# Kernel tuning notes

Hardware: AMD Instinct MI355X
Metric: run time of the kernel (lower is better)

The kernel has to match this reference:

```python
import jax, jax.numpy as jnp
import numpy as np

B, N, C = 32, 577, 1024
NUM_HEADS = 16
HEAD_DIM = C // NUM_HEADS
SCALE = HEAD_DIM ** -0.5
HW = 24          # sqrt(N-1)
POOL = 8         # AdaptiveAvgPool2d output size
KS = HW // POOL  # exact 3x3 average pooling


def setup_inputs() -> dict:
    key = jax.random.key(0)
    k1, k2, k3 = jax.random.split(key, 3)
    X = jax.random.normal(k1, (B, N, C), dtype=jnp.float32)
    W_qkv = jax.random.normal(k2, (3 * C, C), dtype=jnp.float32) * (C ** -0.5)
    W_proj = jax.random.normal(k3, (C, C), dtype=jnp.float32) * (C ** -0.5)
    b_proj = jnp.zeros((C,), dtype=jnp.float32)
    return {"X": X, "W_qkv": W_qkv, "W_proj": W_proj, "b_proj": b_proj, "layer_idx": 1}


def reference(X, W_qkv, W_proj, b_proj, layer_idx):
    # layer_idx <= 100 branch: two-stage pooled-query attention
    qkv = X @ W_qkv.T                              # [B, N, 3C]
    Xq, Xk, Xv = jnp.split(qkv, 3, axis=-1)        # each [B, N, C]

    # Adaptive avg-pool the non-cls query tokens to an 8x8 grid (exact 3x3 mean)
    Qp = Xq[:, :-1, :].reshape(B, POOL, KS, POOL, KS, C).mean(axis=(2, 4))  # [B,8,8,C]
    Qp = Qp.reshape(B, POOL * POOL, C)             # [B, 64, C]

    def to_heads(t, L):
        return t.reshape(B, L, NUM_HEADS, HEAD_DIM).transpose(0, 2, 1, 3)

    Qh = to_heads(Xq, N)       # [B, H, N, d]
    Kh = to_heads(Xk, N)
    Vh = to_heads(Xv, N)
    Q = to_heads(Qp, POOL * POOL)  # [B, H, 64, d]

    # Stage 1: pooled queries cross-attend to full K/V
    s1 = jnp.einsum('bhqd,bhkd->bhqk', Q * SCALE, Kh)   # [B,H,64,N]
    A1 = jax.nn.softmax(s1, axis=-1)
    Q_delta = jnp.einsum('bhqk,bhkd->bhqd', A1, Vh)     # [B,H,64,d]

    # Stage 2: original queries attend to pooled queries, read Q_delta
    s2 = jnp.einsum('bhnd,bhqd->bhnq', Qh * SCALE, Q)   # [B,H,N,64]
    A2 = jax.nn.softmax(s2, axis=-1)
    out = jnp.einsum('bhnq,bhqd->bhnd', A2, Q_delta)    # [B,H,N,d]

    out = out.transpose(0, 2, 1, 3).reshape(B, N, C)
    return out @ W_proj.T + b_proj
```

## Files before the change

### kernel.cpp

```cpp
#include <hip/hip_runtime.h>

typedef unsigned short u16;
typedef u16 u16x8 __attribute__((ext_vector_type(8)));
typedef u16 u16x4 __attribute__((ext_vector_type(4)));
typedef __bf16 bf16x8 __attribute__((ext_vector_type(8)));
typedef float f32x4 __attribute__((ext_vector_type(4)));

#define DEVI static __device__ __forceinline__

#define BB 32
#define NN 577
#define CC 1024
#define HH 16
#define DD 64
#define MM (BB * NN)
#define SCALE_ 0.125f

DEVI u16 f2bf(float f) {
  union { float f; unsigned u; } v; v.f = f;
  unsigned r = v.u + 0x7FFFu + ((v.u >> 16) & 1u);
  return (u16)(r >> 16);
}
DEVI float bf2f(u16 b) {
  union { unsigned u; float f; } v; v.u = ((unsigned)b) << 16; return v.f;
}
DEVI f32x4 mfma16(u16x8 a, u16x8 b, f32x4 c) {
  return __builtin_amdgcn_mfma_f32_16x16x32_bf16(
      __builtin_bit_cast(bf16x8, a), __builtin_bit_cast(bf16x8, b), c, 0, 0, 0);
}
DEVI void gload_lds16(const u16* g, u16* l) {
  __builtin_amdgcn_global_load_lds(
      (const __attribute__((address_space(1))) void*)g,
      (__attribute__((address_space(3))) void*)l, 16, 0, 0);
}

__global__ void cvt_kernel(const float* __restrict__ in, u16* __restrict__ out, int n4) {
  int i = blockIdx.x * blockDim.x + threadIdx.x;
  int stride = gridDim.x * blockDim.x;
  for (; i < n4; i += stride) {
    float4 v = ((const float4*)in)[i];
    u16x4 o = { f2bf(v.x), f2bf(v.y), f2bf(v.z), f2bf(v.w) };
    ((u16x4*)out)[i] = o;
  }
}

__global__ __launch_bounds__(256) void gemm_bt2(
    const u16* __restrict__ A, const u16* __restrict__ Bw,
    u16* __restrict__ Cb, float* __restrict__ Cf, const float* __restrict__ bias,
    int M, int N, int K, int MT, int NT)
{
  __shared__ u16 Als[128 * 64];
  __shared__ u16 Bls[128 * 64];

  int nwg = MT * NT;
  int orig = blockIdx.x;
  int q = nwg >> 3, r = nwg & 7;
  int xcd = orig & 7, idx = orig >> 3;
  int wg = (xcd < r ? xcd * (q + 1) : r * (q + 1) + (xcd - r) * q) + idx;
  int mt = wg / NT, nt = wg % NT;

  const int t = threadIdx.x, lane = t & 63, w = t >> 6;
  const int wr = (w >> 1) * 64, wc = (w & 1) * 64;
  const int fr = lane & 15, fg = lane >> 4;
  const int m0 = mt * 128, n0 = nt * 128;
  f32x4 acc[4][4] = {};

  const int swcol = ((lane & 7) ^ ((lane >> 3) & 7)) * 8;
  const u16* pA[4];
  const u16* pB[4];
#pragma unroll
  for (int i = 0; i < 4; ++i) {
    int row = w * 32 + i * 8 + (lane >> 3);
    int ga = m0 + row; if (ga > M - 1) ga = M - 1;
    pA[i] = A + (size_t)ga * K + swcol;
    pB[i] = Bw + (size_t)(n0 + row) * K + swcol;
  }

  for (int kt = 0; kt < K; kt += 64) {
#pragma unroll
    for (int i = 0; i < 4; ++i) {
      int c = w * 4 + i;
      gload_lds16(pA[i] + kt, &Als[c * 512]);
      gload_lds16(pB[i] + kt, &Bls[c * 512]);
    }
    __syncthreads();
#pragma unroll
    for (int kk = 0; kk < 2; ++kk) {
      u16x8 af[4], bfr[4];
#pragma unroll
      for (int m = 0; m < 4; ++m) {
        int row = wr + m * 16 + fr;
        int ch = (kk * 4 + fg) ^ (fr & 7);
        af[m] = *(const u16x8*)&Als[row * 64 + ch * 8];
      }
#pragma unroll
      for (int n = 0; n < 4; ++n) {
        int row = wc + n * 16 + fr;
        int ch = (kk * 4 + fg) ^ (fr & 7);
        bfr[n] = *(const u16x8*)&Bls[row * 64 + ch * 8];
      }
#pragma unroll
      for (int m = 0; m < 4; ++m)
#pragma unroll
        for (int n = 0; n < 4; ++n)
          acc[m][n] = mfma16(af[m], bfr[n], acc[m][n]);
    }
    __syncthreads();
  }

#pragma unroll
  for (int m = 0; m < 4; ++m) {
#pragma unroll
    for (int j = 0; j < 4; ++j) {
      int row = m0 + wr + m * 16 + fg * 4 + j;
      if (row >= M) continue;
#pragma unroll
      for (int n = 0; n < 4; ++n) {
        int col = n0 + wc + n * 16 + fr;
        float v = acc[m][n][j];
        if (Cf) Cf[(size_t)row * N + col] = v + bias[col];
        else    Cb[(size_t)row * N + col] = f2bf(v);
      }
    }
  }
}

__global__ __launch_bounds__(256) void pool_kernel(const u16* __restrict__ qkv, u16* __restrict__ Qp) {
  int b = blockIdx.x >> 6, pq = blockIdx.x & 63;
  int py = pq >> 3, px = pq & 7;
  int c0 = threadIdx.x * 4;
  float s0 = 0.f, s1 = 0.f, s2 = 0.f, s3 = 0.f;
#pragma unroll
  for (int dy = 0; dy < 3; ++dy)
#pragma unroll
    for (int dx = 0; dx < 3; ++dx) {
      int n = (py * 3 + dy) * 24 + px * 3 + dx;
      u16x4 v = *(const u16x4*)(qkv + (size_t)(b * NN + n) * 3072 + c0);
      s0 += bf2f(v[0]); s1 += bf2f(v[1]); s2 += bf2f(v[2]); s3 += bf2f(v[3]);
    }
  const float r = 1.f / 9.f;
  u16x4 o = { f2bf(s0 * r), f2bf(s1 * r), f2bf(s2 * r), f2bf(s3 * r) };
  *(u16x4*)(Qp + (size_t)(b * 64 + pq) * CC + c0) = o;
}

__global__ __launch_bounds__(256) void stage1_kernel(
    const u16* __restrict__ qkv, const u16* __restrict__ Qp, u16* __restrict__ QdT)
{
  __shared__ u16 Kls[64][72];
  __shared__ u16 Vt[64][72];
  __shared__ u16 Pls[4][16][72];
  int bh = blockIdx.x, b = bh >> 4, h = bh & 15;
  int t = threadIdx.x, lane = t & 63, w = t >> 6;
  int fr = lane & 15, fg = lane >> 4;

  const u16* Qb = Qp + (size_t)(b * 64 + w * 16 + fr) * CC + h * DD;
  u16x8 qf0 = *(const u16x8*)(Qb + fg * 8);
  u16x8 qf1 = *(const u16x8*)(Qb + 32 + fg * 8);

  f32x4 o[4] = {};
  float rowm[4] = {-1e30f, -1e30f, -1e30f, -1e30f};
  float rowl[4] = {};

  for (int kt = 0; kt < 10; ++kt) {
#pragma unroll
    for (int i = 0; i < 2; ++i) {
      int g = t + i * 256;
      int key = g >> 3, cc = (g & 7) * 8;
      int n = kt * 64 + key;
      u16x8 kv = {}, vv = {};
      if (n < NN) {
        const u16* p = qkv + (size_t)(b * NN + n) * 3072 + h * DD + cc;
        kv = *(const u16x8*)(p + CC);
        vv = *(const u16x8*)(p + 2 * CC);
      }
      *(u16x8*)&Kls[key][cc] = kv;
#pragma unroll
      for (int j = 0; j < 8; ++j) Vt[cc + j][key] = vv[j];
    }
    __syncthreads();

    f32x4 s[4] = {};
#pragma unroll
    for (int kk = 0; kk < 2; ++kk) {
      u16x8 qf = kk ? qf1 : qf0;
#pragma unroll
      for (int n = 0; n < 4; ++n) {
        u16x8 kf = *(const u16x8*)&Kls[n * 16 + fr][kk * 32 + fg * 8];
        s[n] = mfma16(qf, kf, s[n]);
      }
    }
    float mx[4] = {-1e30f, -1e30f, -1e30f, -1e30f};
#pragma unroll
    for (int n = 0; n < 4; ++n) {
      int key = kt * 64 + n * 16 + fr;
#pragma unroll
      for (int j = 0; j < 4; ++j) {
        float v = s[n][j] * SCALE_;
        if (key >= NN) v = -1e30f;
        s[n][j] = v;
        mx[j] = fmaxf(mx[j], v);
      }
    }
    for (int d = 1; d < 16; d <<= 1) {
#pragma unroll
      for (int j = 0; j < 4; ++j) mx[j] = fmaxf(mx[j], __shfl_xor(mx[j], d));
    }
    float corr[4];
#pragma unroll
    for (int j = 0; j < 4; ++j) {
      float mn = fmaxf(rowm[j], mx[j]);
      corr[j] = __expf(rowm[j] - mn);
      rowm[j] = mn;
    }
    float rs[4] = {};
#pragma unroll
    for (int n = 0; n < 4; ++n)
#pragma unroll
      for (int j = 0; j < 4; ++j) {
        float p = __expf(s[n][j] - rowm[j]);
        s[n][j] = p;
        rs[j] += p;
      }
    for (int d = 1; d < 16; d <<= 1) {
#pragma unroll
      for (int j = 0; j < 4; ++j) rs[j] += __shfl_xor(rs[j], d);
    }
#pragma unroll
    for (int j = 0; j < 4; ++j) rowl[j] = rowl[j] * corr[j] + rs[j];
#pragma unroll
    for (int n = 0; n < 4; ++n)
#pragma unroll
      for (int j = 0; j < 4; ++j) o[n][j] *= corr[j];

#pragma unroll
    for (int n = 0; n < 4; ++n)
#pragma unroll
      for (int j = 0; j < 4; ++j)
        Pls[w][fg * 4 + j][n * 16 + fr] = f2bf(s[n][j]);
    __syncthreads();

#pragma unroll
    for (int kk = 0; kk < 2; ++kk) {
      u16x8 pf = *(const u16x8*)&Pls[w][fr][kk * 32 + fg * 8];
#pragma unroll
      for (int n = 0; n < 4; ++n) {
        u16x8 vf = *(const u16x8*)&Vt[n * 16 + fr][kk * 32 + fg * 8];
        o[n] = mfma16(pf, vf, o[n]);
      }
    }
    __syncthreads();
  }

#pragma unroll
  for (int n = 0; n < 4; ++n)
#pragma unroll
    for (int j = 0; j < 4; ++j) {
      int dv = n * 16 + fr, q2 = w * 16 + fg * 4 + j;
      QdT[((size_t)bh * 64 + dv) * 64 + q2] = f2bf(o[n][j] / rowl[j]);
    }
}

__global__ __launch_bounds__(256) void stage2_kernel(
    const u16* __restrict__ qkv, const u16* __restrict__ Qp,
    const u16* __restrict__ QdT, u16* __restrict__ AO)
{
  __shared__ u16 Qpl[64][72];
  __shared__ u16 Qdl[64][72];
  __shared__ u16 Pls[4][16][72];
  int id = blockIdx.x;
  int ntile = id % 10;
  int bh = id / 10, b = bh >> 4, h = bh & 15;
  int t = threadIdx.x, lane = t & 63, w = t >> 6;
  int fr = lane & 15, fg = lane >> 4;

#pragma unroll
  for (int i = 0; i < 2; ++i) {
    int g = t + i * 256;
    int row = g >> 3, cc = (g & 7) * 8;
    *(u16x8*)&Qpl[row][cc] = *(const u16x8*)(Qp + (size_t)(b * 64 + row) * CC + h * DD + cc);
    *(u16x8*)&Qdl[row][cc] = *(const u16x8*)(QdT + ((size_t)bh * 64 + row) * 64 + cc);
  }
  __syncthreads();

  int n0 = ntile * 64;
  int qrow = n0 + w * 16 + fr;
  int qc = qrow < NN ? qrow : NN - 1;
  const u16* Qb = qkv + (size_t)(b * NN + qc) * 3072 + h * DD;
  u16x8 qf0 = *(const u16x8*)(Qb + fg * 8);
  u16x8 qf1 = *(const u16x8*)(Qb + 32 + fg * 8);

  f32x4 s[4] = {};
#pragma unroll
  for (int kk = 0; kk < 2; ++kk) {
    u16x8 qf = kk ? qf1 : qf0;
#pragma unroll
    for (int n = 0; n < 4; ++n) {
      u16x8 bfrag = *(const u16x8*)&Qpl[n * 16 + fr][kk * 32 + fg * 8];
      s[n] = mfma16(qf, bfrag, s[n]);
    }
  }
  float mx[4] = {-1e30f, -1e30f, -1e30f, -1e30f};
#pragma unroll
  for (int n = 0; n < 4; ++n)
#pragma unroll
    for (int j = 0; j < 4; ++j) {
      float v = s[n][j] * SCALE_;
      s[n][j] = v;
      mx[j] = fmaxf(mx[j], v);
    }
  for (int d = 1; d < 16; d <<= 1) {
#pragma unroll
    for (int j = 0; j < 4; ++j) mx[j] = fmaxf(mx[j], __shfl_xor(mx[j], d));
  }
  float rs[4] = {};
#pragma unroll
  for (int n = 0; n < 4; ++n)
#pragma unroll
    for (int j = 0; j < 4; ++j) {
      float p = __expf(s[n][j] - mx[j]);
      s[n][j] = p;
      rs[j] += p;
    }
  for (int d = 1; d < 16; d <<= 1) {
#pragma unroll
    for (int j = 0; j < 4; ++j) rs[j] += __shfl_xor(rs[j], d);
  }

#pragma unroll
  for (int n = 0; n < 4; ++n)
#pragma unroll
    for (int j = 0; j < 4; ++j)
      Pls[w][fg * 4 + j][n * 16 + fr] = f2bf(s[n][j]);
  __syncthreads();

  f32x4 of[4] = {};
#pragma unroll
  for (int kk = 0; kk < 2; ++kk) {
    u16x8 pf = *(const u16x8*)&Pls[w][fr][kk * 32 + fg * 8];
#pragma unroll
    for (int n = 0; n < 4; ++n) {
      u16x8 qd = *(const u16x8*)&Qdl[n * 16 + fr][kk * 32 + fg * 8];
      of[n] = mfma16(pf, qd, of[n]);
    }
  }

#pragma unroll
  for (int n = 0; n < 4; ++n)
#pragma unroll
    for (int j = 0; j < 4; ++j) {
      int orow = n0 + w * 16 + fg * 4 + j;
      if (orow < NN)
        AO[(size_t)(b * NN + orow) * CC + h * DD + n * 16 + fr] = f2bf(of[n][j] / rs[j]);
    }
}

extern "C" void kernel_launch(void* const* d_in, const int* in_sizes, int n_in,
                              void* d_out, int out_size, void* d_ws, size_t ws_size,
                              hipStream_t stream) {
  const float* X     = (const float*)d_in[0];
  const float* Wqkv  = (const float*)d_in[1];
  const float* Wproj = (const float*)d_in[2];
  const float* bproj = (const float*)d_in[3];

  char* ws = (char*)d_ws;
  u16* Xb  = (u16*)(ws + 0);
  u16* Wqb = (u16*)(ws + 37814272);
  u16* Wpb = (u16*)(ws + 44105728);
  u16* qkv = (u16*)(ws + 46202880);
  u16* Qpb = (u16*)(ws + 159645696);
  u16* QdT = (u16*)(ws + 163840000);
  u16* AO  = (u16*)(ws + 168034304);

  cvt_kernel<<<2048, 256, 0, stream>>>(X, Xb, (BB * NN * CC) / 4);
  cvt_kernel<<<1024, 256, 0, stream>>>(Wqkv, Wqb, (3 * CC * CC) / 4);
  cvt_kernel<<<512, 256, 0, stream>>>(Wproj, Wpb, (CC * CC) / 4);

  gemm_bt2<<<145 * 24, 256, 0, stream>>>(Xb, Wqb, qkv, nullptr, nullptr,
                                         MM, 3 * CC, CC, 145, 24);

  pool_kernel<<<BB * 64, 256, 0, stream>>>(qkv, Qpb);
  stage1_kernel<<<BB * HH, 256, 0, stream>>>(qkv, Qpb, QdT);
  stage2_kernel<<<BB * HH * 10, 256, 0, stream>>>(qkv, Qpb, QdT, AO);

  gemm_bt2<<<145 * 8, 256, 0, stream>>>(AO, Wpb, nullptr, (float*)d_out, bproj,
                                        MM, CC, CC, 145, 8);
}
```

Before: 302.2 us.

## Double-buffer GEMM with 256x128 tiles, 512 threads, and interleaved prefetch

Replaces the 128x128 single-buffered GEMM with a 256x128 tile computed by 8 waves. LDS is double-buffered, and the global-to-LDS loads for the next k-tile are issued between MFMA groups, with s_setprio raising priority around the MFMA bursts. Each k-step now needs one barrier instead of two, and the larger tile should improve reuse of B and overlap memory with compute. The trade-offs are more LDS use (96KB), fewer workgroups, and tile padding at the M edge (73*256 versus 18464 rows).

After: 383.8 us. +27.0%, slower.

```diff
diff --git a/kernel.cpp b/kernel.cpp
--- a/kernel.cpp
+++ b/kernel.cpp
@@ -44,13 +44,13 @@
   }
 }
 
-__global__ __launch_bounds__(256) void gemm_bt2(
+__global__ __launch_bounds__(512) void gemm_p2(
     const u16* __restrict__ A, const u16* __restrict__ Bw,
     u16* __restrict__ Cb, float* __restrict__ Cf, const float* __restrict__ bias,
     int M, int N, int K, int MT, int NT)
 {
-  __shared__ u16 Als[128 * 64];
-  __shared__ u16 Bls[128 * 64];
+  __shared__ u16 Als[2][256 * 64];
+  __shared__ u16 Bls[2][128 * 64];
 
   int nwg = MT * NT;
   int orig = blockIdx.x;
@@ -60,63 +60,107 @@
   int mt = wg / NT, nt = wg % NT;
 
   const int t = threadIdx.x, lane = t & 63, w = t >> 6;
-  const int wr = (w >> 1) * 64, wc = (w & 1) * 64;
+  const int wr2 = w >> 2, wc2 = w & 3;
   const int fr = lane & 15, fg = lane >> 4;
-  const int m0 = mt * 128, n0 = nt * 128;
-  f32x4 acc[4][4] = {};
+  const int m0 = mt * 256, n0 = nt * 128;
+
+  f32x4 acc[8][2] = {};
 
   const int swcol = ((lane & 7) ^ ((lane >> 3) & 7)) * 8;
   const u16* pA[4];
-  const u16* pB[4];
+  const u16* pB[2];
 #pragma unroll
   for (int i = 0; i < 4; ++i) {
-    int row = w * 32 + i * 8 + (lane >> 3);
+    int row = i * 64 + w * 8 + (lane >> 3);
     int ga = m0 + row; if (ga > M - 1) ga = M - 1;
     pA[i] = A + (size_t)ga * K + swcol;
+  }
+#pragma unroll
+  for (int i = 0; i < 2; ++i) {
+    int row = i * 64 + w * 8 + (lane >> 3);
     pB[i] = Bw + (size_t)(n0 + row) * K + swcol;
   }
 
-  for (int kt = 0; kt < K; kt += 64) {
-#pragma unroll
-    for (int i = 0; i < 4; ++i) {
-      int c = w * 4 + i;
-      gload_lds16(pA[i] + kt, &Als[c * 512]);
-      gload_lds16(pB[i] + kt, &Bls[c * 512]);
+#pragma unroll
+  for (int i = 0; i < 4; ++i) gload_lds16(pA[i], &Als[0][i * 4096 + w * 512]);
+#pragma unroll
+  for (int i = 0; i < 2; ++i) gload_lds16(pB[i], &Bls[0][i * 4096 + w * 512]);
+  __syncthreads();
+
+  const int c0 = (fg ^ (fr & 7)) * 8;
+  const int c1 = ((4 + fg) ^ (fr & 7)) * 8;
+  const int nkt = K >> 6;
+
+  for (int tk = 0; tk < nkt; ++tk) {
+    const int cur = tk & 1, nxt = cur ^ 1;
+    const u16* Ac = &Als[cur][0];
+    const u16* Bc = &Bls[cur][0];
+    const int ktn = (tk + 1) << 6;
+    const bool more = (tk + 1 < nkt);
+
+    if (more) {
+      gload_lds16(pA[0] + ktn, &Als[nxt][0 * 4096 + w * 512]);
+      gload_lds16(pA[1] + ktn, &Als[nxt][1 * 4096 + w * 512]);
+      gload_lds16(pA[2] + ktn, &Als[nxt][2 * 4096 + w * 512]);
+    }
+    u16x8 b00 = *(const u16x8*)&Bc[(wc2 * 32 +  0 + fr) * 64 + c0];
+    u16x8 b01 = *(const u16x8*)&Bc[(wc2 * 32 + 16 + fr) * 64 + c0];
+    u16x8 b10 = *(const u16x8*)&Bc[(wc2 * 32 +  0 + fr) * 64 + c1];
+    u16x8 b11 = *(const u16x8*)&Bc[(wc2 * 32 + 16 + fr) * 64 + c1];
+    {
+      u16x8 a0[4], a1[4];
+#pragma unroll
+      for (int m = 0; m < 4; ++m) {
+        int row = wr2 * 128 + m * 16 + fr;
+        a0[m] = *(const u16x8*)&Ac[row * 64 + c0];
+        a1[m] = *(const u16x8*)&Ac[row * 64 + c1];
+      }
+      __builtin_amdgcn_s_setprio(1);
+#pragma unroll
+      for (int m = 0; m < 4; ++m) {
+        acc[m][0] = mfma16(a0[m], b00, acc[m][0]);
+        acc[m][1] = mfma16(a0[m], b01, acc[m][1]);
+        acc[m][0] = mfma16(a1[m], b10, acc[m][0]);
+        acc[m][1] = mfma16(a1[m], b11, acc[m][1]);
+      }
+      __builtin_amdgcn_s_setprio(0);
+    }
+
+    if (more) {
+      gload_lds16(pA[3] + ktn, &Als[nxt][3 * 4096 + w * 512]);
+      gload_lds16(pB[0] + ktn, &Bls[nxt][0 * 4096 + w * 512]);
+      gload_lds16(pB[1] + ktn, &Bls[nxt][1 * 4096 + w * 512]);
+    }
+    {
+      u16x8 a0[4], a1[4];
+#pragma unroll
+      for (int m = 0; m < 4; ++m) {
+        int row = wr2 * 128 + (m + 4) * 16 + fr;
+        a0[m] = *(const u16x8*)&Ac[row * 64 + c0];
+        a1[m] = *(const u16x8*)&Ac[row * 64 + c1];
+      }
+      __builtin_amdgcn_s_setprio(1);
+#pragma unroll
+      for (int m = 0; m < 4; ++m) {
+        acc[m + 4][0] = mfma16(a0[m], b00, acc[m + 4][0]);
+        acc[m + 4][1] = mfma16(a0[m], b01, acc[m + 4][1]);
+        acc[m + 4][0] = mfma16(a1[m], b10, acc[m + 4][0]);
+        acc[m + 4][1] = mfma16(a1[m], b11, acc[m + 4][1]);
+      }
+      __builtin_amdgcn_s_setprio(0);
     }
     __syncthreads();
-#pragma unroll
-    for (int kk = 0; kk < 2; ++kk) {
-      u16x8 af[4], bfr[4];
-#pragma unroll
-      for (int m = 0; m < 4; ++m) {
-        int row = wr + m * 16 + fr;
-        int ch = (kk * 4 + fg) ^ (fr & 7);
-        af[m] = *(const u16x8*)&Als[row * 64 + ch * 8];
-      }
-#pragma unroll
-      for (int n = 0; n < 4; ++n) {
-        int row = wc + n * 16 + fr;
-        int ch = (kk * 4 + fg) ^ (fr & 7);
-        bfr[n] = *(const u16x8*)&Bls[row * 64 + ch * 8];
-      }
-#pragma unroll
-      for (int m = 0; m < 4; ++m)
-#pragma unroll
-        for (int n = 0; n < 4; ++n)
-          acc[m][n] = mfma16(af[m], bfr[n], acc[m][n]);
-    }
-    __syncthreads();
-  }
-
-#pragma unroll
-  for (int m = 0; m < 4; ++m) {
-#pragma unroll
-    for (int j = 0; j < 4; ++j) {
-      int row = m0 + wr + m * 16 + fg * 4 + j;
+  }
+
+#pragma unroll
+  for (int m = 0; m < 8; ++m) {
+#pragma unroll
+    for (int j = 0; j < 4; ++j) {
+      int row = m0 + wr2 * 128 + m * 16 + fg * 4 + j;
       if (row >= M) continue;
 #pragma unroll
-      for (int n = 0; n < 4; ++n) {
-        int col = n0 + wc + n * 16 + fr;
+      for (int n = 0; n < 2; ++n) {
+        int col = n0 + wc2 * 32 + n * 16 + fr;
         float v = acc[m][n][j];
         if (Cf) Cf[(size_t)row * N + col] = v + bias[col];
         else    Cb[(size_t)row * N + col] = f2bf(v);
@@ -375,13 +419,13 @@
   cvt_kernel<<<1024, 256, 0, stream>>>(Wqkv, Wqb, (3 * CC * CC) / 4);
   cvt_kernel<<<512, 256, 0, stream>>>(Wproj, Wpb, (CC * CC) / 4);
 
-  gemm_bt2<<<145 * 24, 256, 0, stream>>>(Xb, Wqb, qkv, nullptr, nullptr,
-                                         MM, 3 * CC, CC, 145, 24);
+  gemm_p2<<<73 * 24, 512, 0, stream>>>(Xb, Wqb, qkv, nullptr, nullptr,
+                                       MM, 3 * CC, CC, 73, 24);
 
   pool_kernel<<<BB * 64, 256, 0, stream>>>(qkv, Qpb);
   stage1_kernel<<<BB * HH, 256, 0, stream>>>(qkv, Qpb, QdT);
   stage2_kernel<<<BB * HH * 10, 256, 0, stream>>>(qkv, Qpb, QdT, AO);
 
-  gemm_bt2<<<145 * 8, 256, 0, stream>>>(AO, Wpb, nullptr, (float*)d_out, bproj,
-                                        MM, CC, CC, 145, 8);
-}
+  gemm_p2<<<73 * 8, 512, 0, stream>>>(AO, Wpb, nullptr, (float*)d_out, bproj,
+                                      MM, CC, CC, 73, 8);
+}
```

## Replace QKV GEMM with 256x256-tile, 8-wave, four-slot pipelined kernel

Applied to the files above, without the earlier changes.

Adds a new bf16 GEMM for the QKV projection. It uses 256x256 output tiles with 512 threads and a four-slot LDS ring fed by direct global-to-LDS loads, split into half-K stages. MFMA bursts are interleaved with prefetches under explicit barriers and raised wave priority. The goal is more data reuse per tile and better overlap of loads with compute than the previous 128x128 kernel. The cost is large accumulator register pressure, 64KB of LDS per block and fewer blocks. The last row tile is padded, with out-of-range rows clamped on load and skipped on store.

Result: no change. 300.4 us (-0.6%).

```diff
diff --git a/kernel.cpp b/kernel.cpp
--- a/kernel.cpp
+++ b/kernel.cpp
@@ -33,6 +33,11 @@
       (const __attribute__((address_space(1))) void*)g,
       (__attribute__((address_space(3))) void*)l, 16, 0, 0);
 }
+DEVI void bar() {
+  __builtin_amdgcn_sched_barrier(0);
+  __builtin_amdgcn_s_barrier();
+  __builtin_amdgcn_sched_barrier(0);
+}
 
 __global__ void cvt_kernel(const float* __restrict__ in, u16* __restrict__ out, int n4) {
   int i = blockIdx.x * blockDim.x + threadIdx.x;
@@ -41,6 +46,141 @@
     float4 v = ((const float4*)in)[i];
     u16x4 o = { f2bf(v.x), f2bf(v.y), f2bf(v.z), f2bf(v.w) };
     ((u16x4*)out)[i] = o;
+  }
+}
+
+__global__ __launch_bounds__(512, 2) void gemm_p4(
+    const u16* __restrict__ A, const u16* __restrict__ Bw,
+    u16* __restrict__ Cb, int M, int N, int K, int MT, int NT)
+{
+  __shared__ u16 Als[4][8192];
+  __shared__ u16 Bls[4][8192];
+
+  int nwg = MT * NT;
+  int orig = blockIdx.x;
+  int q = nwg >> 3, r = nwg & 7;
+  int xcd = orig & 7, idx = orig >> 3;
+  int wg = (xcd < r ? xcd * (q + 1) : r * (q + 1) + (xcd - r) * q) + idx;
+  int mt = wg / NT, nt = wg % NT;
+
+  const int t = threadIdx.x, lane = t & 63, w = t >> 6;
+  const int wr2 = w >> 2, wc2 = w & 3;
+  const int fr = lane & 15, fg = lane >> 4;
+  const int m0 = mt * 256, n0 = nt * 256;
+
+  f32x4 acc[8][4] = {};
+
+  const int srccol = ((lane & 3) ^ ((lane >> 3) & 3)) * 8;
+  int rA0 = m0 + w * 16 + (lane >> 2);
+  int rA1 = rA0 + 128;
+  if (rA0 > M - 1) rA0 = M - 1;
+  if (rA1 > M - 1) rA1 = M - 1;
+  const u16* pA0 = A + (size_t)rA0 * K + srccol;
+  const u16* pA1 = A + (size_t)rA1 * K + srccol;
+  const u16* pB0 = Bw + (size_t)(n0 + w * 16 + (lane >> 2)) * K + srccol;
+  const u16* pB1 = pB0 + (size_t)128 * K;
+  const int ldsoff = w * 512;
+
+  auto stageA = [&](int tile, int kh, int slot) {
+    const int col = tile * 64 + kh * 32;
+    gload_lds16(pA0 + col, &Als[slot][ldsoff]);
+    gload_lds16(pA1 + col, &Als[slot][4096 + ldsoff]);
+  };
+  auto stageB = [&](int tile, int kh, int slot) {
+    const int col = tile * 64 + kh * 32;
+    gload_lds16(pB0 + col, &Bls[slot][ldsoff]);
+    gload_lds16(pB1 + col, &Bls[slot][4096 + ldsoff]);
+  };
+
+  const int swch8 = (fg ^ ((fr >> 1) & 3)) * 8;
+  const int aoff = (wr2 * 128 + fr) * 32 + swch8;
+  const int boff = (wc2 * 64 + fr) * 32 + swch8;
+
+  const int nkt = K >> 6;
+
+  stageA(0, 0, 0); stageB(0, 0, 0);
+  stageA(0, 1, 1); stageB(0, 1, 1);
+  stageA(1, 0, 2); stageB(1, 0, 2);
+  asm volatile("s_waitcnt vmcnt(8)" ::: "memory");
+  bar();
+
+  for (int tk = 0; tk < nkt; ++tk) {
+    const int s0 = (2 * tk) & 3, s1 = (2 * tk + 1) & 3, s3 = (2 * tk + 3) & 3;
+    const int t1 = (tk + 1 < nkt) ? tk + 1 : 0;
+    const int t2 = (tk + 2 < nkt) ? tk + 2 : tk + 2 - nkt;
+    u16x8 a[4], b[4];
+
+#pragma unroll
+    for (int m = 0; m < 4; ++m) a[m] = *(const u16x8*)&Als[s0][aoff + m * 512];
+#pragma unroll
+    for (int n = 0; n < 4; ++n) b[n] = *(const u16x8*)&Bls[s0][boff + n * 512];
+    stageA(t1, 1, s3);
+    bar();
+    __builtin_amdgcn_s_setprio(1);
+#pragma unroll
+    for (int m = 0; m < 4; ++m)
+#pragma unroll
+      for (int n = 0; n < 4; ++n)
+        acc[m][n] = mfma16(a[m], b[n], acc[m][n]);
+    __builtin_amdgcn_s_setprio(0);
+    bar();
+
+#pragma unroll
+    for (int m = 0; m < 4; ++m) a[m] = *(const u16x8*)&Als[s0][aoff + (m + 4) * 512];
+    stageB(t1, 1, s3);
+    bar();
+    __builtin_amdgcn_s_setprio(1);
+#pragma unroll
+    for (int m = 0; m < 4; ++m)
+#pragma unroll
+      for (int n = 0; n < 4; ++n)
+        acc[m + 4][n] = mfma16(a[m], b[n], acc[m + 4][n]);
+    __builtin_amdgcn_s_setprio(0);
+    asm volatile("s_waitcnt vmcnt(8)" ::: "memory");
+    bar();
+
+#pragma unroll
+    for (int m = 0; m < 4; ++m) a[m] = *(const u16x8*)&Als[s1][aoff + m * 512];
+#pragma unroll
+    for (int n = 0; n < 4; ++n) b[n] = *(const u16x8*)&Bls[s1][boff + n * 512];
+    stageA(t2, 0, s0);
+    bar();
+    __builtin_amdgcn_s_setprio(1);
+#pragma unroll
+    for (int m = 0; m < 4; ++m)
+#pragma unroll
+      for (int n = 0; n < 4; ++n)
+        acc[m][n] = mfma16(a[m], b[n], acc[m][n]);
+    __builtin_amdgcn_s_setprio(0);
+    bar();
+
+#pragma unroll
+    for (int m = 0; m < 4; ++m) a[m] = *(const u16x8*)&Als[s1][aoff + (m + 4) * 512];
+    stageB(t2, 0, s0);
+    bar();
+    __builtin_amdgcn_s_setprio(1);
+#pragma unroll
+    for (int m = 0; m < 4; ++m)
+#pragma unroll
+      for (int n = 0; n < 4; ++n)
+        acc[m + 4][n] = mfma16(a[m], b[n], acc[m + 4][n]);
+    __builtin_amdgcn_s_setprio(0);
+    asm volatile("s_waitcnt vmcnt(8)" ::: "memory");
+    bar();
+  }
+
+#pragma unroll
+  for (int m = 0; m < 8; ++m) {
+#pragma unroll
+    for (int j = 0; j < 4; ++j) {
+      int row = m0 + wr2 * 128 + m * 16 + fg * 4 + j;
+      if (row >= M) continue;
+#pragma unroll
+      for (int n = 0; n < 4; ++n) {
+        int col = n0 + wc2 * 64 + n * 16 + fr;
+        Cb[(size_t)row * N + col] = f2bf(acc[m][n][j]);
+      }
+    }
   }
 }
 
@@ -375,8 +515,7 @@
   cvt_kernel<<<1024, 256, 0, stream>>>(Wqkv, Wqb, (3 * CC * CC) / 4);
   cvt_kernel<<<512, 256, 0, stream>>>(Wproj, Wpb, (CC * CC) / 4);
 
-  gemm_bt2<<<145 * 24, 256, 0, stream>>>(Xb, Wqb, qkv, nullptr, nullptr,
-                                         MM, 3 * CC, CC, 145, 24);
+  gemm_p4<<<73 * 12, 512, 0, stream>>>(Xb, Wqb, qkv, MM, 3 * CC, CC, 73, 12);
 
   pool_kernel<<<BB * 64, 256, 0, stream>>>(qkv, Qpb);
   stage1_kernel<<<BB * HH, 256, 0, stream>>>(qkv, Qpb, QdT);
```

## Fuse pooling, stage-1 and stage-2 attention into one per-head kernel; merge conversions

Applied to the files above, without the earlier changes.

Pooling, stage-1 cross-attention and stage-2 attention now run in one kernel, one block per (batch, head). Pooled queries and Q_delta stay in shared memory instead of going through global buffers, which removes two launches and the intermediate global traffic. The three fp32-to-bf16 conversion launches are merged into a single grid-stride kernel. In exchange, stage 2 runs serially in 10 tiles inside 512 blocks rather than across 5120 blocks, which lowers parallelism for that phase.

After: 298.3 us. No clear change (-1.3%).

```diff
diff --git a/kernel.cpp b/kernel.cpp
--- a/kernel.cpp
+++ b/kernel.cpp
@@ -34,13 +34,23 @@
       (__attribute__((address_space(3))) void*)l, 16, 0, 0);
 }
 
-__global__ void cvt_kernel(const float* __restrict__ in, u16* __restrict__ out, int n4) {
+__global__ void cvt3_kernel(const float* __restrict__ X, const float* __restrict__ Wq,
+                            const float* __restrict__ Wp, u16* __restrict__ Xb,
+                            u16* __restrict__ Wqb, u16* __restrict__ Wpb) {
+  const int nX = (MM * CC) / 4;
+  const int nQ = (3 * CC * CC) / 4;
+  const int nP = (CC * CC) / 4;
+  const int total = nX + nQ + nP;
   int i = blockIdx.x * blockDim.x + threadIdx.x;
   int stride = gridDim.x * blockDim.x;
-  for (; i < n4; i += stride) {
-    float4 v = ((const float4*)in)[i];
+  for (; i < total; i += stride) {
+    const float* in; u16* out; int k;
+    if (i < nX)            { in = X;  out = Xb;  k = i; }
+    else if (i < nX + nQ)  { in = Wq; out = Wqb; k = i - nX; }
+    else                   { in = Wp; out = Wpb; k = i - nX - nQ; }
+    float4 v = ((const float4*)in)[k];
     u16x4 o = { f2bf(v.x), f2bf(v.y), f2bf(v.z), f2bf(v.w) };
-    ((u16x4*)out)[i] = o;
+    ((u16x4*)out)[k] = o;
   }
 }
 
@@ -125,99 +135,191 @@
   }
 }
 
-__global__ __launch_bounds__(256) void pool_kernel(const u16* __restrict__ qkv, u16* __restrict__ Qp) {
-  int b = blockIdx.x >> 6, pq = blockIdx.x & 63;
-  int py = pq >> 3, px = pq & 7;
-  int c0 = threadIdx.x * 4;
-  float s0 = 0.f, s1 = 0.f, s2 = 0.f, s3 = 0.f;
-#pragma unroll
-  for (int dy = 0; dy < 3; ++dy)
-#pragma unroll
-    for (int dx = 0; dx < 3; ++dx) {
-      int n = (py * 3 + dy) * 24 + px * 3 + dx;
-      u16x4 v = *(const u16x4*)(qkv + (size_t)(b * NN + n) * 3072 + c0);
-      s0 += bf2f(v[0]); s1 += bf2f(v[1]); s2 += bf2f(v[2]); s3 += bf2f(v[3]);
-    }
-  const float r = 1.f / 9.f;
-  u16x4 o = { f2bf(s0 * r), f2bf(s1 * r), f2bf(s2 * r), f2bf(s3 * r) };
-  *(u16x4*)(Qp + (size_t)(b * 64 + pq) * CC + c0) = o;
-}
-
-__global__ __launch_bounds__(256) void stage1_kernel(
-    const u16* __restrict__ qkv, const u16* __restrict__ Qp, u16* __restrict__ QdT)
+__global__ __launch_bounds__(256) void attn_fused(
+    const u16* __restrict__ qkv, u16* __restrict__ AO)
 {
+  __shared__ u16 Qp[64][72];
+  __shared__ u16 Qd[64][72];
   __shared__ u16 Kls[64][72];
   __shared__ u16 Vt[64][72];
   __shared__ u16 Pls[4][16][72];
+
   int bh = blockIdx.x, b = bh >> 4, h = bh & 15;
   int t = threadIdx.x, lane = t & 63, w = t >> 6;
   int fr = lane & 15, fg = lane >> 4;
 
-  const u16* Qb = Qp + (size_t)(b * 64 + w * 16 + fr) * CC + h * DD;
-  u16x8 qf0 = *(const u16x8*)(Qb + fg * 8);
-  u16x8 qf1 = *(const u16x8*)(Qb + 32 + fg * 8);
-
-  f32x4 o[4] = {};
-  float rowm[4] = {-1e30f, -1e30f, -1e30f, -1e30f};
-  float rowl[4] = {};
-
-  for (int kt = 0; kt < 10; ++kt) {
-#pragma unroll
-    for (int i = 0; i < 2; ++i) {
-      int g = t + i * 256;
-      int key = g >> 3, cc = (g & 7) * 8;
-      int n = kt * 64 + key;
-      u16x8 kv = {}, vv = {};
-      if (n < NN) {
-        const u16* p = qkv + (size_t)(b * NN + n) * 3072 + h * DD + cc;
-        kv = *(const u16x8*)(p + CC);
-        vv = *(const u16x8*)(p + 2 * CC);
-      }
-      *(u16x8*)&Kls[key][cc] = kv;
-#pragma unroll
-      for (int j = 0; j < 8; ++j) Vt[cc + j][key] = vv[j];
-    }
-    __syncthreads();
+  {
+    int pq = t >> 2, d0 = (t & 3) * 16;
+    int py = pq >> 3, px = pq & 7;
+    float s[16] = {};
+#pragma unroll
+    for (int dy = 0; dy < 3; ++dy)
+#pragma unroll
+      for (int dx = 0; dx < 3; ++dx) {
+        int n = (py * 3 + dy) * 24 + px * 3 + dx;
+        const u16* p = qkv + (size_t)(b * NN + n) * 3072 + h * DD + d0;
+        u16x8 v0 = *(const u16x8*)p;
+        u16x8 v1 = *(const u16x8*)(p + 8);
+#pragma unroll
+        for (int j = 0; j < 8; ++j) { s[j] += bf2f(v0[j]); s[8 + j] += bf2f(v1[j]); }
+      }
+    const float rinv = 1.f / 9.f;
+    u16x8 o0, o1;
+#pragma unroll
+    for (int j = 0; j < 8; ++j) { o0[j] = f2bf(s[j] * rinv); o1[j] = f2bf(s[8 + j] * rinv); }
+    *(u16x8*)&Qp[pq][d0] = o0;
+    *(u16x8*)&Qp[pq][d0 + 8] = o1;
+  }
+  __syncthreads();
+
+  {
+    u16x8 qf0 = *(const u16x8*)&Qp[w * 16 + fr][fg * 8];
+    u16x8 qf1 = *(const u16x8*)&Qp[w * 16 + fr][32 + fg * 8];
+
+    f32x4 o[4] = {};
+    float rowm[4] = {-1e30f, -1e30f, -1e30f, -1e30f};
+    float rowl[4] = {};
+
+    for (int kt = 0; kt < 10; ++kt) {
+#pragma unroll
+      for (int i = 0; i < 2; ++i) {
+        int g = t + i * 256;
+        int key = g >> 3, cc = (g & 7) * 8;
+        int n = kt * 64 + key;
+        u16x8 kv = {}, vv = {};
+        if (n < NN) {
+          const u16* p = qkv + (size_t)(b * NN + n) * 3072 + h * DD + cc;
+          kv = *(const u16x8*)(p + CC);
+          vv = *(const u16x8*)(p + 2 * CC);
+        }
+        *(u16x8*)&Kls[key][cc] = kv;
+#pragma unroll
+        for (int j = 0; j < 8; ++j) Vt[cc + j][key] = vv[j];
+      }
+      __syncthreads();
+
+      f32x4 s[4] = {};
+#pragma unroll
+      for (int kk = 0; kk < 2; ++kk) {
+        u16x8 qf = kk ? qf1 : qf0;
+#pragma unroll
+        for (int n = 0; n < 4; ++n) {
+          u16x8 kf = *(const u16x8*)&Kls[n * 16 + fr][kk * 32 + fg * 8];
+          s[n] = mfma16(qf, kf, s[n]);
+        }
+      }
+      float mx[4] = {-1e30f, -1e30f, -1e30f, -1e30f};
+#pragma unroll
+      for (int n = 0; n < 4; ++n) {
+        int key = kt * 64 + n * 16 + fr;
+#pragma unroll
+        for (int j = 0; j < 4; ++j) {
+          float v = s[n][j] * SCALE_;
+          if (key >= NN) v = -1e30f;
+          s[n][j] = v;
+          mx[j] = fmaxf(mx[j], v);
+        }
+      }
+      for (int d = 1; d < 16; d <<= 1) {
+#pragma unroll
+        for (int j = 0; j < 4; ++j) mx[j] = fmaxf(mx[j], __shfl_xor(mx[j], d));
+      }
+      float corr[4];
+#pragma unroll
+      for (int j = 0; j < 4; ++j) {
+        float mn = fmaxf(rowm[j], mx[j]);
+        corr[j] = __expf(rowm[j] - mn);
+        rowm[j] = mn;
+      }
+      float rs[4] = {};
+#pragma unroll
+      for (int n = 0; n < 4; ++n)
+#pragma unroll
+        for (int j = 0; j < 4; ++j) {
+          float p = __expf(s[n][j] - rowm[j]);
+          s[n][j] = p;
+          rs[j] += p;
+        }
+      for (int d = 1; d < 16; d <<= 1) {
+#pragma unroll
+        for (int j = 0; j < 4; ++j) rs[j] += __shfl_xor(rs[j], d);
+      }
+#pragma unroll
+      for (int j = 0; j < 4; ++j) rowl[j] = rowl[j] * corr[j] + rs[j];
+#pragma unroll
+      for (int n = 0; n < 4; ++n)
+#pragma unroll
+        for (int j = 0; j < 4; ++j) o[n][j] *= corr[j];
+
+#pragma unroll
+      for (int n = 0; n < 4; ++n)
+#pragma unroll
+        for (int j = 0; j < 4; ++j)
+          Pls[w][fg * 4 + j][n * 16 + fr] = f2bf(s[n][j]);
+      __syncthreads();
+
+#pragma unroll
+      for (int kk = 0; kk < 2; ++kk) {
+        u16x8 pf = *(const u16x8*)&Pls[w][fr][kk * 32 + fg * 8];
+#pragma unroll
+        for (int n = 0; n < 4; ++n) {
+          u16x8 vf = *(const u16x8*)&Vt[n * 16 + fr][kk * 32 + fg * 8];
+          o[n] = mfma16(pf, vf, o[n]);
+        }
+      }
+      __syncthreads();
+    }
+
+#pragma unroll
+    for (int n = 0; n < 4; ++n)
+#pragma unroll
+      for (int j = 0; j < 4; ++j)
+        Qd[n * 16 + fr][w * 16 + fg * 4 + j] = f2bf(o[n][j] / rowl[j]);
+  }
+  __syncthreads();
+
+  u16x8 bq[2][4], dq[2][4];
+#pragma unroll
+  for (int kk = 0; kk < 2; ++kk)
+#pragma unroll
+    for (int n = 0; n < 4; ++n) {
+      bq[kk][n] = *(const u16x8*)&Qp[n * 16 + fr][kk * 32 + fg * 8];
+      dq[kk][n] = *(const u16x8*)&Qd[n * 16 + fr][kk * 32 + fg * 8];
+    }
+
+  for (int nt = 0; nt < 10; ++nt) {
+    int n0 = nt * 64;
+    int qrow = n0 + w * 16 + fr;
+    int qc = qrow < NN ? qrow : NN - 1;
+    const u16* Qb = qkv + (size_t)(b * NN + qc) * 3072 + h * DD;
+    u16x8 a0 = *(const u16x8*)(Qb + fg * 8);
+    u16x8 a1 = *(const u16x8*)(Qb + 32 + fg * 8);
 
     f32x4 s[4] = {};
 #pragma unroll
-    for (int kk = 0; kk < 2; ++kk) {
-      u16x8 qf = kk ? qf1 : qf0;
-#pragma unroll
-      for (int n = 0; n < 4; ++n) {
-        u16x8 kf = *(const u16x8*)&Kls[n * 16 + fr][kk * 32 + fg * 8];
-        s[n] = mfma16(qf, kf, s[n]);
-      }
+    for (int n = 0; n < 4; ++n) {
+      s[n] = mfma16(a0, bq[0][n], s[n]);
+      s[n] = mfma16(a1, bq[1][n], s[n]);
     }
     float mx[4] = {-1e30f, -1e30f, -1e30f, -1e30f};
 #pragma unroll
-    for (int n = 0; n < 4; ++n) {
-      int key = kt * 64 + n * 16 + fr;
+    for (int n = 0; n < 4; ++n)
 #pragma unroll
       for (int j = 0; j < 4; ++j) {
         float v = s[n][j] * SCALE_;
-        if (key >= NN) v = -1e30f;
         s[n][j] = v;
         mx[j] = fmaxf(mx[j], v);
       }
-    }
     for (int d = 1; d < 16; d <<= 1) {
 #pragma unroll
       for (int j = 0; j < 4; ++j) mx[j] = fmaxf(mx[j], __shfl_xor(mx[j], d));
     }
-    float corr[4];
-#pragma unroll
-    for (int j = 0; j < 4; ++j) {
-      float mn = fmaxf(rowm[j], mx[j]);
-      corr[j] = __expf(rowm[j] - mn);
-      rowm[j] = mn;
-    }
     float rs[4] = {};
 #pragma unroll
     for (int n = 0; n < 4; ++n)
 #pragma unroll
       for (int j = 0; j < 4; ++j) {
-        float p = __expf(s[n][j] - rowm[j]);
+        float p = __expf(s[n][j] - mx[j]);
         s[n][j] = p;
         rs[j] += p;
       }
@@ -225,12 +327,6 @@
 #pragma unroll
       for (int j = 0; j < 4; ++j) rs[j] += __shfl_xor(rs[j], d);
     }
-#pragma unroll
-    for (int j = 0; j < 4; ++j) rowl[j] = rowl[j] * corr[j] + rs[j];
-#pragma unroll
-    for (int n = 0; n < 4; ++n)
-#pragma unroll
-      for (int j = 0; j < 4; ++j) o[n][j] *= corr[j];
 
 #pragma unroll
     for (int n = 0; n < 4; ++n)
@@ -239,119 +335,25 @@
         Pls[w][fg * 4 + j][n * 16 + fr] = f2bf(s[n][j]);
     __syncthreads();
 
+    f32x4 of[4] = {};
 #pragma unroll
     for (int kk = 0; kk < 2; ++kk) {
       u16x8 pf = *(const u16x8*)&Pls[w][fr][kk * 32 + fg * 8];
 #pragma unroll
-      for (int n = 0; n < 4; ++n) {
-        u16x8 vf = *(const u16x8*)&Vt[n * 16 + fr][kk * 32 + fg * 8];
-        o[n] = mfma16(pf, vf, o[n]);
-      }
-    }
+      for (int n = 0; n < 4; ++n)
+        of[n] = mfma16(pf, dq[kk][n], of[n]);
+    }
+
+#pragma unroll
+    for (int n = 0; n < 4; ++n)
+#pragma unroll
+      for (int j = 0; j < 4; ++j) {
+        int orow = n0 + w * 16 + fg * 4 + j;
+        if (orow < NN)
+          AO[(size_t)(b * NN + orow) * CC + h * DD + n * 16 + fr] = f2bf(of[n][j] / rs[j]);
+      }
     __syncthreads();
   }
-
-#pragma unroll
-  for (int n = 0; n < 4; ++n)
-#pragma unroll
-    for (int j = 0; j < 4; ++j) {
-      int dv = n * 16 + fr, q2 = w * 16 + fg * 4 + j;
-      QdT[((size_t)bh * 64 + dv) * 64 + q2] = f2bf(o[n][j] / rowl[j]);
-    }
-}
-
-__global__ __launch_bounds__(256) void stage2_kernel(
-    const u16* __restrict__ qkv, const u16* __restrict__ Qp,
-    const u16* __restrict__ QdT, u16* __restrict__ AO)
-{
-  __shared__ u16 Qpl[64][72];
-  __shared__ u16 Qdl[64][72];
-  __shared__ u16 Pls[4][16][72];
-  int id = blockIdx.x;
-  int ntile = id % 10;
-  int bh = id / 10, b = bh >> 4, h = bh & 15;
-  int t = threadIdx.x, lane = t & 63, w = t >> 6;
-  int fr = lane & 15, fg = lane >> 4;
-
-#pragma unroll
-  for (int i = 0; i < 2; ++i) {
-    int g = t + i * 256;
-    int row = g >> 3, cc = (g & 7) * 8;
-    *(u16x8*)&Qpl[row][cc] = *(const u16x8*)(Qp + (size_t)(b * 64 + row) * CC + h * DD + cc);
-    *(u16x8*)&Qdl[row][cc] = *(const u16x8*)(QdT + ((size_t)bh * 64 + row) * 64 + cc);
-  }
-  __syncthreads();
-
-  int n0 = ntile * 64;
-  int qrow = n0 + w * 16 + fr;
-  int qc = qrow < NN ? qrow : NN - 1;
-  const u16* Qb = qkv + (size_t)(b * NN + qc) * 3072 + h * DD;
-  u16x8 qf0 = *(const u16x8*)(Qb + fg * 8);
-  u16x8 qf1 = *(const u16x8*)(Qb + 32 + fg * 8);
-
-  f32x4 s[4] = {};
-#pragma unroll
-  for (int kk = 0; kk < 2; ++kk) {
-    u16x8 qf = kk ? qf1 : qf0;
-#pragma unroll
-    for (int n = 0; n < 4; ++n) {
-      u16x8 bfrag = *(const u16x8*)&Qpl[n * 16 + fr][kk * 32 + fg * 8];
-      s[n] = mfma16(qf, bfrag, s[n]);
-    }
-  }
-  float mx[4] = {-1e30f, -1e30f, -1e30f, -1e30f};
-#pragma unroll
-  for (int n = 0; n < 4; ++n)
-#pragma unroll
-    for (int j = 0; j < 4; ++j) {
-      float v = s[n][j] * SCALE_;
-      s[n][j] = v;
-      mx[j] = fmaxf(mx[j], v);
-    }
-  for (int d = 1; d < 16; d <<= 1) {
-#pragma unroll
-    for (int j = 0; j < 4; ++j) mx[j] = fmaxf(mx[j], __shfl_xor(mx[j], d));
-  }
-  float rs[4] = {};
-#pragma unroll
-  for (int n = 0; n < 4; ++n)
-#pragma unroll
-    for (int j = 0; j < 4; ++j) {
-      float p = __expf(s[n][j] - mx[j]);
-      s[n][j] = p;
-      rs[j] += p;
-    }
-  for (int d = 1; d < 16; d <<= 1) {
-#pragma unroll
-    for (int j = 0; j < 4; ++j) rs[j] += __shfl_xor(rs[j], d);
-  }
-
-#pragma unroll
-  for (int n = 0; n < 4; ++n)
-#pragma unroll
-    for (int j = 0; j < 4; ++j)
-      Pls[w][fg * 4 + j][n * 16 + fr] = f2bf(s[n][j]);
-  __syncthreads();
-
-  f32x4 of[4] = {};
-#pragma unroll
-  for (int kk = 0; kk < 2; ++kk) {
-    u16x8 pf = *(const u16x8*)&Pls[w][fr][kk * 32 + fg * 8];
-#pragma unroll
-    for (int n = 0; n < 4; ++n) {
-      u16x8 qd = *(const u16x8*)&Qdl[n * 16 + fr][kk * 32 + fg * 8];
-      of[n] = mfma16(pf, qd, of[n]);
-    }
-  }
-
-#pragma unroll
-  for (int n = 0; n < 4; ++n)
-#pragma unroll
-    for (int j = 0; j < 4; ++j) {
-      int orow = n0 + w * 16 + fg * 4 + j;
-      if (orow < NN)
-        AO[(size_t)(b * NN + orow) * CC + h * DD + n * 16 + fr] = f2bf(of[n][j] / rs[j]);
-    }
 }
 
 extern "C" void kernel_launch(void* const* d_in, const int* in_sizes, int n_in,
@@ -367,20 +369,14 @@
   u16* Wqb = (u16*)(ws + 37814272);
   u16* Wpb = (u16*)(ws + 44105728);
   u16* qkv = (u16*)(ws + 46202880);
-  u16* Qpb = (u16*)(ws + 159645696);
-  u16* QdT = (u16*)(ws + 163840000);
-  u16* AO  = (u16*)(ws + 168034304);
-
-  cvt_kernel<<<2048, 256, 0, stream>>>(X, Xb, (BB * NN * CC) / 4);
-  cvt_kernel<<<1024, 256, 0, stream>>>(Wqkv, Wqb, (3 * CC * CC) / 4);
-  cvt_kernel<<<512, 256, 0, stream>>>(Wproj, Wpb, (CC * CC) / 4);
+  u16* AO  = (u16*)(ws + 159645696);
+
+  cvt3_kernel<<<2048, 256, 0, stream>>>(X, Wqkv, Wproj, Xb, Wqb, Wpb);
 
   gemm_bt2<<<145 * 24, 256, 0, stream>>>(Xb, Wqb, qkv, nullptr, nullptr,
                                          MM, 3 * CC, CC, 145, 24);
 
-  pool_kernel<<<BB * 64, 256, 0, stream>>>(qkv, Qpb);
-  stage1_kernel<<<BB * HH, 256, 0, stream>>>(qkv, Qpb, QdT);
-  stage2_kernel<<<BB * HH * 10, 256, 0, stream>>>(qkv, Qpb, QdT, AO);
+  attn_fused<<<BB * HH, 256, 0, stream>>>(qkv, AO);
 
   gemm_bt2<<<145 * 8, 256, 0, stream>>>(AO, Wpb, nullptr, (float*)d_out, bproj,
                                         MM, CC, CC, 145, 8);
```
